# Kernel tuning notes

Hardware: AMD Instinct MI355X
Metric: run time of the kernel (lower is better)

The kernel has to match this reference:

```python
import jax, jax.numpy as jnp
import numpy as np

N = 4096
IN_DIM = 6
HID = 32
HEADS1 = 4
OUT_DIM = 64


def _gat_layer(x, mask, W, a_src, a_dst, b):
    # x: [n, in], W: [in, heads*d], a_src/a_dst: [heads, d], b: [heads*d]
    n = x.shape[0]
    heads, d = a_src.shape
    h = (x @ W).reshape(n, heads, d)                      # [n, heads, d]
    e_src = jnp.einsum('nhd,hd->nh', h, a_src)            # [n, heads]
    e_dst = jnp.einsum('nhd,hd->nh', h, a_dst)            # [n, heads]
    logits = e_src[:, None, :] + e_dst[None, :, :]        # [n, n, heads]
    logits = jax.nn.leaky_relu(logits, negative_slope=0.2)
    logits = jnp.where(mask[:, :, None], logits, jnp.float32(-1e9))
    alpha = jax.nn.softmax(logits, axis=1)                # softmax over j (dim=1)
    # dropout disabled (eval mode reference)
    out = jnp.einsum('ijh,jhd->ihd', alpha, h).reshape(n, heads * d)
    return out + b


def setup_inputs() -> dict:
    key = jax.random.key(0)
    ks = jax.random.split(key, 10)
    x = jax.random.normal(ks[0], (N, IN_DIM), dtype=jnp.float32)
    adj = jax.random.bernoulli(ks[1], 0.01, (N, N)).astype(jnp.float32)
    s = 0.1
    W1 = jax.random.normal(ks[2], (IN_DIM, HEADS1 * HID), dtype=jnp.float32) * s
    a_src1 = jax.random.normal(ks[3], (HEADS1, HID), dtype=jnp.float32) * s
    a_dst1 = jax.random.normal(ks[4], (HEADS1, HID), dtype=jnp.float32) * s
    b1 = jnp.zeros((HEADS1 * HID,), dtype=jnp.float32)
    W2 = jax.random.normal(ks[5], (HEADS1 * HID, OUT_DIM), dtype=jnp.float32) * s
    a_src2 = jax.random.normal(ks[6], (1, OUT_DIM), dtype=jnp.float32) * s
    a_dst2 = jax.random.normal(ks[7], (1, OUT_DIM), dtype=jnp.float32) * s
    b2 = jnp.zeros((OUT_DIM,), dtype=jnp.float32)
    return {'x': x, 'adj': adj, 'W1': W1, 'a_src1': a_src1, 'a_dst1': a_dst1,
            'b1': b1, 'W2': W2, 'a_src2': a_src2, 'a_dst2': a_dst2, 'b2': b2}


def reference(x, adj, W1, a_src1, a_dst1, b1, W2, a_src2, a_dst2, b2):
    n = x.shape[0]
    # add self loops: a = max(a, I), mask = a > 0
    a = jnp.maximum(adj, jnp.eye(n, dtype=adj.dtype))
    mask = a > 0
    h1 = jax.nn.elu(_gat_layer(x, mask, W1, a_src1, a_dst1, b1))
    # dropout disabled (eval mode)
    h2 = _gat_layer(h1, mask, W2, a_src2, a_dst2, b2)
    return h2
```

## Files before the change

kernel.cpp:

```cpp
#include <hip/hip_runtime.h>

#define N 4096
#define IN_DIM 6
#define HEADS1 4
#define D1 128
#define OUT_DIM 64
#define MAXNB 192

#define WFENCE() do { asm volatile("s_waitcnt lgkmcnt(0)" ::: "memory"); \
                      __builtin_amdgcn_sched_barrier(0); } while (0)

__device__ __forceinline__ float lrelu(float v) { return v > 0.f ? v : 0.2f * v; }
__device__ __forceinline__ float selh(float4 v, int h) {
    return (h == 0) ? v.x : (h == 1) ? v.y : (h == 2) ? v.z : v.w;
}

__global__ __launch_bounds__(256) void kA(
    const float* __restrict__ x,  const float* __restrict__ W1,
    const float* __restrict__ a_src1, const float* __restrict__ a_dst1,
    const float* __restrict__ W2,
    float* __restrict__ hpre, float* __restrict__ es1, float* __restrict__ ed1,
    float* __restrict__ W2T)
{
    int w = threadIdx.x >> 6, l = threadIdx.x & 63;
    int i = blockIdx.x * 4 + w;

    float xv[IN_DIM];
    #pragma unroll
    for (int k = 0; k < IN_DIM; ++k) xv[k] = x[i*IN_DIM + k];

    float a0 = 0.f, a1 = 0.f;
    #pragma unroll
    for (int k = 0; k < IN_DIM; ++k) {
        float2 wv = ((const float2*)W1)[k*64 + l];
        a0 += xv[k] * wv.x;
        a1 += xv[k] * wv.y;
    }
    float2 hv; hv.x = a0; hv.y = a1;
    ((float2*)hpre)[(size_t)i*64 + l] = hv;

    float2 asv = ((const float2*)a_src1)[l];
    float2 adv = ((const float2*)a_dst1)[l];
    float ps = a0*asv.x + a1*asv.y;
    float pd = a0*adv.x + a1*adv.y;
    #pragma unroll
    for (int off = 8; off >= 1; off >>= 1) {
        ps += __shfl_xor(ps, off, 64);
        pd += __shfl_xor(pd, off, 64);
    }
    if ((l & 15) == 0) {
        int h = l >> 4;
        es1[i*HEADS1 + h] = ps;
        ed1[i*HEADS1 + h] = pd;
    }

    if (blockIdx.x == 0) {
        for (int idx = threadIdx.x; idx < D1*OUT_DIM; idx += 256) {
            int k = idx >> 6, o = idx & 63;
            W2T[o*D1 + k] = W2[idx];
        }
    }
}

__global__ __launch_bounds__(256, 4) void kB(
    const float* __restrict__ adj,  const float* __restrict__ hpre,
    const float* __restrict__ es1,  const float* __restrict__ ed1,
    const float* __restrict__ b1,   const float* __restrict__ W2T,
    const float* __restrict__ a_src2, const float* __restrict__ a_dst2,
    int* __restrict__ cnt, int* __restrict__ idxg,
    float* __restrict__ h2pre, float* __restrict__ es2, float* __restrict__ ed2)
{
    __shared__ int   jsS[4][MAXNB];
    __shared__ float lgS[4][HEADS1][MAXNB];
    __shared__ float h1S[4][D1];
    int w = threadIdx.x >> 6, l = threadIdx.x & 63;
    int i = blockIdx.x * 4 + w;
    int*   js  = jsS[w];
    float (*lg)[MAXNB] = lgS[w];
    float* h1s = h1S[w];

    const float4* row = (const float4*)(adj + (size_t)i * N);
    unsigned long long lanem = (1ull << l) - 1ull;
    int base = 0;
    float4 buf[4];
    #pragma unroll
    for (int u = 0; u < 4; ++u) buf[u] = row[l + 64*u];
    #pragma unroll
    for (int ch = 0; ch < 4; ++ch) {
        float4 nbuf[4];
        if (ch < 3) {
            #pragma unroll
            for (int u = 0; u < 4; ++u) nbuf[u] = row[l + 64*u + 256*(ch+1)];
        }
        #pragma unroll
        for (int u = 0; u < 4; ++u) {
            float fe[4] = {buf[u].x, buf[u].y, buf[u].z, buf[u].w};
            #pragma unroll
            for (int e = 0; e < 4; ++e) {
                int j = (256*ch + 64*u + l)*4 + e;
                bool pred = (fe[e] > 0.f) || (j == i);
                unsigned long long mask = __ballot(pred);
                if (pred) {
                    int pos = base + (int)__popcll(mask & lanem);
                    if (pos < MAXNB) js[pos] = j;
                }
                base += (int)__popcll(mask);
            }
        }
        if (ch < 3) {
            #pragma unroll
            for (int u = 0; u < 4; ++u) buf[u] = nbuf[u];
        }
    }
    int c = min(base, MAXNB);
    if (l == 0) cnt[i] = c;
    WFENCE();

    float4 esv = ((const float4*)es1)[i];
    float4 lr0, lr1, lr2;
    lr0.x = lr0.y = lr0.z = lr0.w = -1e30f; lr1 = lr0; lr2 = lr0;
    if (l < c) {
        int j = js[l];
        float4 e4 = ((const float4*)ed1)[j];
        lr0.x = lrelu(esv.x + e4.x); lr0.y = lrelu(esv.y + e4.y);
        lr0.z = lrelu(esv.z + e4.z); lr0.w = lrelu(esv.w + e4.w);
        lg[0][l] = lr0.x; lg[1][l] = lr0.y; lg[2][l] = lr0.z; lg[3][l] = lr0.w;
        idxg[i*MAXNB + l] = j;
    }
    if (l + 64 < c) {
        int p = l + 64, j = js[p];
        float4 e4 = ((const float4*)ed1)[j];
        lr1.x = lrelu(esv.x + e4.x); lr1.y = lrelu(esv.y + e4.y);
        lr1.z = lrelu(esv.z + e4.z); lr1.w = lrelu(esv.w + e4.w);
        lg[0][p] = lr1.x; lg[1][p] = lr1.y; lg[2][p] = lr1.z; lg[3][p] = lr1.w;
        idxg[i*MAXNB + p] = j;
    }
    if (l + 128 < c) {
        int p = l + 128, j = js[p];
        float4 e4 = ((const float4*)ed1)[j];
        lr2.x = lrelu(esv.x + e4.x); lr2.y = lrelu(esv.y + e4.y);
        lr2.z = lrelu(esv.z + e4.z); lr2.w = lrelu(esv.w + e4.w);
        lg[0][p] = lr2.x; lg[1][p] = lr2.y; lg[2][p] = lr2.z; lg[3][p] = lr2.w;
        idxg[i*MAXNB + p] = j;
    }

    float4 mm;
    mm.x = fmaxf(lr0.x, fmaxf(lr1.x, lr2.x));
    mm.y = fmaxf(lr0.y, fmaxf(lr1.y, lr2.y));
    mm.z = fmaxf(lr0.z, fmaxf(lr1.z, lr2.z));
    mm.w = fmaxf(lr0.w, fmaxf(lr1.w, lr2.w));
    #pragma unroll
    for (int off = 32; off >= 1; off >>= 1) {
        mm.x = fmaxf(mm.x, __shfl_xor(mm.x, off, 64));
        mm.y = fmaxf(mm.y, __shfl_xor(mm.y, off, 64));
        mm.z = fmaxf(mm.z, __shfl_xor(mm.z, off, 64));
        mm.w = fmaxf(mm.w, __shfl_xor(mm.w, off, 64));
    }
    float4 ss;
    ss.x = __expf(lr0.x-mm.x) + __expf(lr1.x-mm.x) + __expf(lr2.x-mm.x);
    ss.y = __expf(lr0.y-mm.y) + __expf(lr1.y-mm.y) + __expf(lr2.y-mm.y);
    ss.z = __expf(lr0.z-mm.z) + __expf(lr1.z-mm.z) + __expf(lr2.z-mm.z);
    ss.w = __expf(lr0.w-mm.w) + __expf(lr1.w-mm.w) + __expf(lr2.w-mm.w);
    #pragma unroll
    for (int off = 32; off >= 1; off >>= 1) {
        ss.x += __shfl_xor(ss.x, off, 64);
        ss.y += __shfl_xor(ss.y, off, 64);
        ss.z += __shfl_xor(ss.z, off, 64);
        ss.w += __shfl_xor(ss.w, off, 64);
    }
    WFENCE();

    int hl = l >> 4;
    float m   = selh(mm, hl);
    float inv = 1.f / selh(ss, hl);
    const float2* hp2 = (const float2*)hpre;
    float ax = 0.f, ay = 0.f;
    int p = 0;
    for (; p + 8 <= c; p += 8) {
        int   jj[8]; float ww[8];
        #pragma unroll
        for (int u = 0; u < 8; ++u) jj[u] = js[p+u];
        #pragma unroll
        for (int u = 0; u < 8; ++u) ww[u] = __expf(lg[hl][p+u] - m);
        #pragma unroll
        for (int u = 0; u < 8; ++u) {
            float2 v = hp2[(size_t)jj[u]*64 + l];
            ax += ww[u]*v.x; ay += ww[u]*v.y;
        }
    }
    for (; p < c; ++p) {
        float wv = __expf(lg[hl][p] - m);
        float2 v = hp2[(size_t)js[p]*64 + l];
        ax += wv*v.x; ay += wv*v.y;
    }
    float2 bv = ((const float2*)b1)[l];
    float v0 = ax*inv + bv.x, v1 = ay*inv + bv.y;
    v0 = (v0 > 0.f) ? v0 : expm1f(v0);
    v1 = (v1 > 0.f) ? v1 : expm1f(v1);
    { float2 hw; hw.x = v0; hw.y = v1; *(float2*)(h1s + 2*l) = hw; }
    WFENCE();

    const float4* wrow = (const float4*)(W2T + (size_t)l*D1);
    float h2 = 0.f;
    #pragma unroll 8
    for (int k4 = 0; k4 < 32; ++k4) {
        float4 wv = wrow[k4];
        float4 hvv = *(const float4*)(h1s + k4*4);
        h2 += wv.x*hvv.x + wv.y*hvv.y + wv.z*hvv.z + wv.w*hvv.w;
    }
    h2pre[(size_t)i*OUT_DIM + l] = h2;
    float ps = h2 * a_src2[l];
    float pd = h2 * a_dst2[l];
    #pragma unroll
    for (int off = 32; off >= 1; off >>= 1) {
        ps += __shfl_xor(ps, off, 64);
        pd += __shfl_xor(pd, off, 64);
    }
    if (l == 0) { es2[i] = ps; ed2[i] = pd; }
}

__global__ __launch_bounds__(256, 6) void kC(
    const float* __restrict__ h2pre, const float* __restrict__ es2,
    const float* __restrict__ ed2,   const int* __restrict__ cnt,
    const int* __restrict__ idxg,    const float* __restrict__ b2v,
    float* __restrict__ out)
{
    __shared__ int   jsS[4][MAXNB];
    __shared__ float alS[4][MAXNB];
    int w = threadIdx.x >> 6, l = threadIdx.x & 63;
    int i = blockIdx.x * 4 + w;
    int*   js = jsS[w];
    float* al = alS[w];
    int c = cnt[i];
    float esi = es2[i];

    float l0 = -1e30f, l1 = -1e30f, l2 = -1e30f;
    if (l < c) {
        int j = idxg[i*MAXNB + l];            js[l] = j;
        float v = lrelu(esi + ed2[j]);        al[l] = v;  l0 = v;
    }
    if (l + 64 < c) {
        int p = l + 64, j = idxg[i*MAXNB + p]; js[p] = j;
        float v = lrelu(esi + ed2[j]);         al[p] = v;  l1 = v;
    }
    if (l + 128 < c) {
        int p = l + 128, j = idxg[i*MAXNB + p]; js[p] = j;
        float v = lrelu(esi + ed2[j]);          al[p] = v;  l2 = v;
    }
    float m = fmaxf(l0, fmaxf(l1, l2));
    #pragma unroll
    for (int off = 32; off >= 1; off >>= 1) m = fmaxf(m, __shfl_xor(m, off, 64));
    float s = __expf(l0-m) + __expf(l1-m) + __expf(l2-m);
    #pragma unroll
    for (int off = 32; off >= 1; off >>= 1) s += __shfl_xor(s, off, 64);
    float inv = 1.f / s;
    WFENCE();

    float acc = 0.f;
    int p = 0;
    for (; p + 8 <= c; p += 8) {
        int   jj[8]; float ww[8];
        #pragma unroll
        for (int u = 0; u < 8; ++u) jj[u] = js[p+u];
        #pragma unroll
        for (int u = 0; u < 8; ++u) ww[u] = __expf(al[p+u] - m);
        #pragma unroll
        for (int u = 0; u < 8; ++u)
            acc += ww[u] * h2pre[(size_t)jj[u]*OUT_DIM + l];
    }
    for (; p < c; ++p)
        acc += __expf(al[p] - m) * h2pre[(size_t)js[p]*OUT_DIM + l];
    out[(size_t)i*OUT_DIM + l] = acc*inv + b2v[l];
}

extern "C" void kernel_launch(void* const* d_in, const int* in_sizes, int n_in,
                              void* d_out, int out_size, void* d_ws, size_t ws_size,
                              hipStream_t stream) {
    const float* x      = (const float*)d_in[0];
    const float* adj    = (const float*)d_in[1];
    const float* W1     = (const float*)d_in[2];
    const float* a_src1 = (const float*)d_in[3];
    const float* a_dst1 = (const float*)d_in[4];
    const float* b1     = (const float*)d_in[5];
    const float* W2     = (const float*)d_in[6];
    const float* a_src2 = (const float*)d_in[7];
    const float* a_dst2 = (const float*)d_in[8];
    const float* b2v    = (const float*)d_in[9];
    float* out = (float*)d_out;

    float* ws    = (float*)d_ws;
    float* hpre  = ws;
    float* h2pre = hpre  + (size_t)N*D1;
    float* es1   = h2pre + (size_t)N*OUT_DIM;
    float* ed1   = es1   + (size_t)N*HEADS1;
    float* es2   = ed1   + (size_t)N*HEADS1;
    float* ed2   = es2   + N;
    float* W2T   = ed2   + N;
    int*   cnt   = (int*)(W2T + OUT_DIM*D1);
    int*   idxg  = cnt + N;

    kA<<<N/4, 256, 0, stream>>>(x, W1, a_src1, a_dst1, W2, hpre, es1, ed1, W2T);
    kB<<<N/4, 256, 0, stream>>>(adj, hpre, es1, ed1, b1, W2T, a_src2, a_dst2,
                                cnt, idxg, h2pre, es2, ed2);
    kC<<<N/4, 256, 0, stream>>>(h2pre, es2, ed2, cnt, idxg, b2v, out);
}
```

Baseline: 147.4 us.

## Issue all adjacency loads up front and store normalized softmax weights in LDS

In kB, the whole 4096-float adjacency row is now loaded per lane (16 float4) before the ballot compaction, replacing the double-buffered chunked loop, so memory-level parallelism goes up at the cost of more registers. Both kB and kC now keep the exponentials computed during the softmax reduction, normalize them once, and store the final attention weights in LDS. This removes the repeated exp and scale in the gather loops. kB's LDS row stride is padded to 200, and kC's launch bound drops its min-blocks hint from 6 to 4.

```diff
diff --git a/kernel.cpp b/kernel.cpp
--- a/kernel.cpp
+++ b/kernel.cpp
@@ -6,6 +6,7 @@
 #define D1 128
 #define OUT_DIM 64
 #define MAXNB 192
+#define LGS 200
 
 #define WFENCE() do { asm volatile("s_waitcnt lgkmcnt(0)" ::: "memory"); \
                       __builtin_amdgcn_sched_barrier(0); } while (0)
@@ -71,45 +72,35 @@
     float* __restrict__ h2pre, float* __restrict__ es2, float* __restrict__ ed2)
 {
     __shared__ int   jsS[4][MAXNB];
-    __shared__ float lgS[4][HEADS1][MAXNB];
+    __shared__ float lgS[4][HEADS1][LGS];
     __shared__ float h1S[4][D1];
     int w = threadIdx.x >> 6, l = threadIdx.x & 63;
     int i = blockIdx.x * 4 + w;
     int*   js  = jsS[w];
-    float (*lg)[MAXNB] = lgS[w];
+    float (*lg)[LGS] = lgS[w];
     float* h1s = h1S[w];
 
     const float4* row = (const float4*)(adj + (size_t)i * N);
+    float4 buf[16];
+    #pragma unroll
+    for (int u = 0; u < 16; ++u) buf[u] = row[l + 64*u];
+    __builtin_amdgcn_sched_barrier(0);
+
     unsigned long long lanem = (1ull << l) - 1ull;
     int base = 0;
-    float4 buf[4];
-    #pragma unroll
-    for (int u = 0; u < 4; ++u) buf[u] = row[l + 64*u];
-    #pragma unroll
-    for (int ch = 0; ch < 4; ++ch) {
-        float4 nbuf[4];
-        if (ch < 3) {
-            #pragma unroll
-            for (int u = 0; u < 4; ++u) nbuf[u] = row[l + 64*u + 256*(ch+1)];
-        }
-        #pragma unroll
-        for (int u = 0; u < 4; ++u) {
-            float fe[4] = {buf[u].x, buf[u].y, buf[u].z, buf[u].w};
-            #pragma unroll
-            for (int e = 0; e < 4; ++e) {
-                int j = (256*ch + 64*u + l)*4 + e;
-                bool pred = (fe[e] > 0.f) || (j == i);
-                unsigned long long mask = __ballot(pred);
-                if (pred) {
-                    int pos = base + (int)__popcll(mask & lanem);
-                    if (pos < MAXNB) js[pos] = j;
-                }
-                base += (int)__popcll(mask);
+    #pragma unroll
+    for (int u = 0; u < 16; ++u) {
+        float fe[4] = {buf[u].x, buf[u].y, buf[u].z, buf[u].w};
+        #pragma unroll
+        for (int e = 0; e < 4; ++e) {
+            int j = (64*u + l)*4 + e;
+            bool pred = (fe[e] > 0.f) || (j == i);
+            unsigned long long mask = __ballot(pred);
+            if (pred) {
+                int pos = base + (int)__popcll(mask & lanem);
+                if (pos < MAXNB) js[pos] = j;
             }
-        }
-        if (ch < 3) {
-            #pragma unroll
-            for (int u = 0; u < 4; ++u) buf[u] = nbuf[u];
+            base += (int)__popcll(mask);
         }
     }
     int c = min(base, MAXNB);
@@ -124,7 +115,6 @@
         float4 e4 = ((const float4*)ed1)[j];
         lr0.x = lrelu(esv.x + e4.x); lr0.y = lrelu(esv.y + e4.y);
         lr0.z = lrelu(esv.z + e4.z); lr0.w = lrelu(esv.w + e4.w);
-        lg[0][l] = lr0.x; lg[1][l] = lr0.y; lg[2][l] = lr0.z; lg[3][l] = lr0.w;
         idxg[i*MAXNB + l] = j;
     }
     if (l + 64 < c) {
@@ -132,7 +122,6 @@
         float4 e4 = ((const float4*)ed1)[j];
         lr1.x = lrelu(esv.x + e4.x); lr1.y = lrelu(esv.y + e4.y);
         lr1.z = lrelu(esv.z + e4.z); lr1.w = lrelu(esv.w + e4.w);
-        lg[0][p] = lr1.x; lg[1][p] = lr1.y; lg[2][p] = lr1.z; lg[3][p] = lr1.w;
         idxg[i*MAXNB + p] = j;
     }
     if (l + 128 < c) {
@@ -140,7 +129,6 @@
         float4 e4 = ((const float4*)ed1)[j];
         lr2.x = lrelu(esv.x + e4.x); lr2.y = lrelu(esv.y + e4.y);
         lr2.z = lrelu(esv.z + e4.z); lr2.w = lrelu(esv.w + e4.w);
-        lg[0][p] = lr2.x; lg[1][p] = lr2.y; lg[2][p] = lr2.z; lg[3][p] = lr2.w;
         idxg[i*MAXNB + p] = j;
     }
 
@@ -156,11 +144,18 @@
         mm.z = fmaxf(mm.z, __shfl_xor(mm.z, off, 64));
         mm.w = fmaxf(mm.w, __shfl_xor(mm.w, off, 64));
     }
+    float4 ex0, ex1, ex2;
+    ex0.x = __expf(lr0.x-mm.x); ex0.y = __expf(lr0.y-mm.y);
+    ex0.z = __expf(lr0.z-mm.z); ex0.w = __expf(lr0.w-mm.w);
+    ex1.x = __expf(lr1.x-mm.x); ex1.y = __expf(lr1.y-mm.y);
+    ex1.z = __expf(lr1.z-mm.z); ex1.w = __expf(lr1.w-mm.w);
+    ex2.x = __expf(lr2.x-mm.x); ex2.y = __expf(lr2.y-mm.y);
+    ex2.z = __expf(lr2.z-mm.z); ex2.w = __expf(lr2.w-mm.w);
     float4 ss;
-    ss.x = __expf(lr0.x-mm.x) + __expf(lr1.x-mm.x) + __expf(lr2.x-mm.x);
-    ss.y = __expf(lr0.y-mm.y) + __expf(lr1.y-mm.y) + __expf(lr2.y-mm.y);
-    ss.z = __expf(lr0.z-mm.z) + __expf(lr1.z-mm.z) + __expf(lr2.z-mm.z);
-    ss.w = __expf(lr0.w-mm.w) + __expf(lr1.w-mm.w) + __expf(lr2.w-mm.w);
+    ss.x = ex0.x + ex1.x + ex2.x;
+    ss.y = ex0.y + ex1.y + ex2.y;
+    ss.z = ex0.z + ex1.z + ex2.z;
+    ss.w = ex0.w + ex1.w + ex2.w;
     #pragma unroll
     for (int off = 32; off >= 1; off >>= 1) {
         ss.x += __shfl_xor(ss.x, off, 64);
@@ -168,11 +163,16 @@
         ss.z += __shfl_xor(ss.z, off, 64);
         ss.w += __shfl_xor(ss.w, off, 64);
     }
+    float4 iv; iv.x = 1.f/ss.x; iv.y = 1.f/ss.y; iv.z = 1.f/ss.z; iv.w = 1.f/ss.w;
+    lg[0][l]     = ex0.x*iv.x; lg[1][l]     = ex0.y*iv.y;
+    lg[2][l]     = ex0.z*iv.z; lg[3][l]     = ex0.w*iv.w;
+    lg[0][l+64]  = ex1.x*iv.x; lg[1][l+64]  = ex1.y*iv.y;
+    lg[2][l+64]  = ex1.z*iv.z; lg[3][l+64]  = ex1.w*iv.w;
+    lg[0][l+128] = ex2.x*iv.x; lg[1][l+128] = ex2.y*iv.y;
+    lg[2][l+128] = ex2.z*iv.z; lg[3][l+128] = ex2.w*iv.w;
     WFENCE();
 
     int hl = l >> 4;
-    float m   = selh(mm, hl);
-    float inv = 1.f / selh(ss, hl);
     const float2* hp2 = (const float2*)hpre;
     float ax = 0.f, ay = 0.f;
     int p = 0;
@@ -181,7 +181,7 @@
         #pragma unroll
         for (int u = 0; u < 8; ++u) jj[u] = js[p+u];
         #pragma unroll
-        for (int u = 0; u < 8; ++u) ww[u] = __expf(lg[hl][p+u] - m);
+        for (int u = 0; u < 8; ++u) ww[u] = lg[hl][p+u];
         #pragma unroll
         for (int u = 0; u < 8; ++u) {
             float2 v = hp2[(size_t)jj[u]*64 + l];
@@ -189,12 +189,12 @@
         }
     }
     for (; p < c; ++p) {
-        float wv = __expf(lg[hl][p] - m);
+        float wv = lg[hl][p];
         float2 v = hp2[(size_t)js[p]*64 + l];
         ax += wv*v.x; ay += wv*v.y;
     }
     float2 bv = ((const float2*)b1)[l];
-    float v0 = ax*inv + bv.x, v1 = ay*inv + bv.y;
+    float v0 = ax + bv.x, v1 = ay + bv.y;
     v0 = (v0 > 0.f) ? v0 : expm1f(v0);
     v1 = (v1 > 0.f) ? v1 : expm1f(v1);
     { float2 hw; hw.x = v0; hw.y = v1; *(float2*)(h1s + 2*l) = hw; }
@@ -219,7 +219,7 @@
     if (l == 0) { es2[i] = ps; ed2[i] = pd; }
 }
 
-__global__ __launch_bounds__(256, 6) void kC(
+__global__ __launch_bounds__(256, 4) void kC(
     const float* __restrict__ h2pre, const float* __restrict__ es2,
     const float* __restrict__ ed2,   const int* __restrict__ cnt,
     const int* __restrict__ idxg,    const float* __restrict__ b2v,
@@ -236,24 +236,28 @@
 
     float l0 = -1e30f, l1 = -1e30f, l2 = -1e30f;
     if (l < c) {
-        int j = idxg[i*MAXNB + l];            js[l] = j;
-        float v = lrelu(esi + ed2[j]);        al[l] = v;  l0 = v;
+        int j = idxg[i*MAXNB + l];             js[l] = j;
+        l0 = lrelu(esi + ed2[j]);
     }
     if (l + 64 < c) {
         int p = l + 64, j = idxg[i*MAXNB + p]; js[p] = j;
-        float v = lrelu(esi + ed2[j]);         al[p] = v;  l1 = v;
+        l1 = lrelu(esi + ed2[j]);
     }
     if (l + 128 < c) {
         int p = l + 128, j = idxg[i*MAXNB + p]; js[p] = j;
-        float v = lrelu(esi + ed2[j]);          al[p] = v;  l2 = v;
+        l2 = lrelu(esi + ed2[j]);
     }
     float m = fmaxf(l0, fmaxf(l1, l2));
     #pragma unroll
     for (int off = 32; off >= 1; off >>= 1) m = fmaxf(m, __shfl_xor(m, off, 64));
-    float s = __expf(l0-m) + __expf(l1-m) + __expf(l2-m);
+    float e0 = __expf(l0-m), e1 = __expf(l1-m), e2 = __expf(l2-m);
+    float s = e0 + e1 + e2;
     #pragma unroll
     for (int off = 32; off >= 1; off >>= 1) s += __shfl_xor(s, off, 64);
     float inv = 1.f / s;
+    al[l]     = e0*inv;
+    al[l+64]  = e1*inv;
+    al[l+128] = e2*inv;
     WFENCE();
 
     float acc = 0.f;
@@ -263,14 +267,14 @@
         #pragma unroll
         for (int u = 0; u < 8; ++u) jj[u] = js[p+u];
         #pragma unroll
-        for (int u = 0; u < 8; ++u) ww[u] = __expf(al[p+u] - m);
+        for (int u = 0; u < 8; ++u) ww[u] = al[p+u];
         #pragma unroll
         for (int u = 0; u < 8; ++u)
             acc += ww[u] * h2pre[(size_t)jj[u]*OUT_DIM + l];
     }
     for (; p < c; ++p)
-        acc += __expf(al[p] - m) * h2pre[(size_t)js[p]*OUT_DIM + l];
-    out[(size_t)i*OUT_DIM + l] = acc*inv + b2v[l];
+        acc += al[p] * h2pre[(size_t)js[p]*OUT_DIM + l];
+    out[(size_t)i*OUT_DIM + l] = acc + b2v[l];
 }
 
 extern "C" void kernel_launch(void* const* d_in, const int* in_sizes, int n_in,
```

Measured after the change: 144.7 us. Within noise of the previous version (-1.9%).
